# Optimization experiments

Measured on AMD Instinct MI355X. Metric: run time of the kernel, lower is better.

Reference implementation:

```python
import jax, jax.numpy as jnp
import numpy as np

B, N, D, H = 16, 576, 768, 8
HD = D // H
SCALE = HD ** -0.5
EPS = 1e-5  # torch LayerNorm default


def _ln(x, g, b):
    mu = jnp.mean(x, axis=-1, keepdims=True)
    var = jnp.mean(jnp.square(x - mu), axis=-1, keepdims=True)
    return (x - mu) * jax.lax.rsqrt(var + EPS) * g + b


def setup_inputs() -> dict:
    key = jax.random.key(0)
    ks = jax.random.split(key, 20)
    s = D ** -0.5
    inp = {
        "x1": jax.random.normal(ks[0], (B, N, D), jnp.float32),
        "x2": jax.random.normal(ks[1], (B, N, D), jnp.float32),
        # projection weights stored [in, out]
        "Wq": jax.random.normal(ks[2], (D, D), jnp.float32) * s,
        "bq": jnp.zeros((D,), jnp.float32),
        "Wk": jax.random.normal(ks[3], (D, D), jnp.float32) * s,
        "bk": jnp.zeros((D,), jnp.float32),
        "Wv": jax.random.normal(ks[4], (D, D), jnp.float32) * s,
        "bv": jnp.zeros((D,), jnp.float32),
        "Wo": jax.random.normal(ks[5], (D, D), jnp.float32) * s,
        "bo": jnp.zeros((D,), jnp.float32),
        "g1": jnp.ones((D,), jnp.float32),
        "be1": jnp.zeros((D,), jnp.float32),
        "g2": jnp.ones((D,), jnp.float32),
        "be2": jnp.zeros((D,), jnp.float32),
        "W1": jax.random.normal(ks[6], (D, 4 * D), jnp.float32) * s,
        "bf1": jnp.zeros((4 * D,), jnp.float32),
        "W2": jax.random.normal(ks[7], (4 * D, D), jnp.float32) * (4 * D) ** -0.5,
        "bf2": jnp.zeros((D,), jnp.float32),
    }
    return inp


def reference(x1, x2, Wq, bq, Wk, bk, Wv, bv, Wo, bo, g1, be1, g2, be2, W1, bf1, W2, bf2):
    def heads(x, W, b):
        # [B,N,D] -> [B,H,N,HD]
        return (x @ W + b).reshape(B, N, H, HD).transpose(0, 2, 1, 3)

    def block(xq, xkv):
        q = heads(xq, Wq, bq)
        k = heads(xkv, Wk, bk)
        v = heads(xkv, Wv, bv)
        attn = jax.nn.softmax(jnp.einsum('bhqd,bhkd->bhqk', q, k) * SCALE, axis=-1)
        o = jnp.einsum('bhqk,bhkd->bqhd', attn, v).reshape(B, N, D)
        o = o @ Wo + bo
        h = _ln(xq + o, g1, be1)
        f = jax.nn.gelu(h @ W1 + bf1, approximate=False) @ W2 + bf2
        return _ln(h + f, g2, be2), attn

    out1, a1 = block(x1, x2)
    out2, a2 = block(x2, x1)
    attn_map = (a1 + a2.transpose(0, 1, 3, 2)) * 0.5
    return out1, out2, attn_map
```

## Files before the change

kernel.cpp:

```cpp
#include <hip/hip_runtime.h>
#include <cstdint>
#include <cstddef>

#define B_   16
#define N_   576
#define D_   768
#define H_   8
#define HD_  96
#define DF_  3072
#define R_   (B_*N_)
#define SCALE_F 0.10206207261596575f

typedef __bf16 bf16;
typedef __attribute__((ext_vector_type(8))) __bf16 bf16x8;
typedef __attribute__((ext_vector_type(4))) __bf16 bf16x4;
typedef __attribute__((ext_vector_type(4))) float  f32x4;

__device__ __forceinline__ void gld_lds16(const void* g, void* l) {
  __builtin_amdgcn_global_load_lds((const __attribute__((address_space(1))) void*)g,
                                   (__attribute__((address_space(3))) void*)l,
                                   16, 0, 0);
}
__device__ __forceinline__ void nt_f32(float* p, float v) { __builtin_nontemporal_store(v, p); }
__device__ __forceinline__ void nt_u64(void* p, unsigned long long v) { __builtin_nontemporal_store(v, (unsigned long long*)p); }
__device__ __forceinline__ void nt_bf16(bf16* p, float v) {
  bf16 h = (bf16)v; unsigned short u; __builtin_memcpy(&u, &h, 2);
  __builtin_nontemporal_store(u, (unsigned short*)p);
}
__device__ __forceinline__ float gelu_f(float v) {
  float u = 0.7978845608028654f * v * (1.0f + 0.044715f*v*v);
  float e = __expf(2.0f*u);
  float th = 1.0f - 2.0f/(e + 1.0f);
  return 0.5f*v*(1.0f + th);
}

__global__ void cast_f32_bf16_k(const float* __restrict__ x, bf16* __restrict__ y, int n4) {
  int i = blockIdx.x*256 + threadIdx.x;
  if (i >= n4) return;
  f32x4 v = ((const f32x4*)x)[i];
  union { bf16 h[4]; unsigned long long q; } u;
  u.h[0] = (bf16)v[0]; u.h[1] = (bf16)v[1]; u.h[2] = (bf16)v[2]; u.h[3] = (bf16)v[3];
  nt_u64((unsigned long long*)y + i, u.q);
}

__global__ void transpose_cast_k(const float* __restrict__ W, bf16* __restrict__ WT,
                                 int rows, int cols) {
  __shared__ float tile[32][33];
  int cb = blockIdx.x*32, rb = blockIdx.y*32;
  int tx = threadIdx.x, ty = threadIdx.y;
  #pragma unroll
  for (int i=0;i<32;i+=8)
    tile[ty+i][tx] = W[(size_t)(rb+ty+i)*cols + cb+tx];
  __syncthreads();
  #pragma unroll
  for (int i=0;i<32;i+=8)
    WT[(size_t)(cb+ty+i)*rows + rb+tx] = (bf16)tile[tx][ty+i];
}

__global__ void concat_bias_k(const float* a, const float* b, const float* c, float* o) {
  int i = blockIdx.x*256 + threadIdx.x;
  if (i < 768) o[i] = a[i];
  else if (i < 1536) o[i] = b[i-768];
  else if (i < 2304) o[i] = c[i-1536];
}

template<int EPI, int SWZ>
__global__ __launch_bounds__(512, 2) void gemm256_k(
    const bf16* __restrict__ A, const bf16* __restrict__ Bt,
    const float* __restrict__ bias,
    bf16* __restrict__ outB, bf16* __restrict__ outK, bf16* __restrict__ outVT,
    int Nn, int K, int nct)
{
  __shared__ __align__(16) char lds[65536];
  const int t = threadIdx.x;
  const int lane = t & 63, w = t >> 6, g = lane >> 4, r = lane & 15;
  const int wr = w >> 2, wc = w & 3;

  const int cpx = gridDim.x >> 3;
  const int xcd = blockIdx.x & 7, loc = blockIdx.x >> 3;
  int rt, ct;
  if (SWZ) {
    const int nrt_x = cpx / nct;
    ct = loc / nrt_x;
    rt = xcd * nrt_x + (loc - ct*nrt_x);
  } else {
    const int wg = xcd*cpx + loc;
    rt = wg / nct; ct = wg - rt*nct;
  }
  const size_t a0 = (size_t)rt*256, b0 = (size_t)ct*256;

  f32x4 acc[8][4];
  #pragma unroll
  for (int m=0;m<8;++m)
    #pragma unroll
    for (int n=0;n<4;++n) acc[m][n] = (f32x4){0.f,0.f,0.f,0.f};

  const int rbase = ((t>>6)<<4) + (t&15);
  const int kbase = ((t>>4)&3)*8;
  const bf16* Ab = A  + (a0 + rbase)*(size_t)K + kbase;
  const bf16* Bb = Bt + (b0 + rbase)*(size_t)K + kbase;
  const size_t rstep = (size_t)128*K;
  char* Al = lds + t*16;
  char* Bl = lds + 32768 + t*16;

#define STAGE256(tt, cc) do { \
    const size_t ko_ = (size_t)(tt)*32; \
    gld_lds16(Ab + ko_,         Al + (cc)*16384); \
    gld_lds16(Ab + rstep + ko_, Al + (cc)*16384 + 8192); \
    gld_lds16(Bb + ko_,         Bl + (cc)*16384); \
    gld_lds16(Bb + rstep + ko_, Bl + (cc)*16384 + 8192); \
  } while (0)

  const int NT = K >> 5;
  STAGE256(0, 0);
  for (int tt = 0; tt < NT; ++tt) {
    const int c = tt & 1;
    if (tt + 1 < NT) {
      STAGE256(tt + 1, c ^ 1);
      asm volatile("s_waitcnt vmcnt(4)" ::: "memory");
    } else {
      asm volatile("s_waitcnt vmcnt(0)" ::: "memory");
    }
    __builtin_amdgcn_sched_barrier(0);
    __builtin_amdgcn_s_barrier();
    __builtin_amdgcn_sched_barrier(0);

    const char* Ard = lds + c*16384 + (wr<<13) + lane*16;
    const char* Brd = lds + 32768 + c*16384 + (wc<<12) + lane*16;
    bf16x8 bfr[4], af[4];
    #pragma unroll
    for (int n=0;n<4;++n) bfr[n] = *(const bf16x8*)(Brd + n*1024);
    #pragma unroll
    for (int m=0;m<4;++m) af[m]  = *(const bf16x8*)(Ard + m*1024);
    __builtin_amdgcn_s_setprio(1);
    #pragma unroll
    for (int m=0;m<4;++m)
      #pragma unroll
      for (int n=0;n<4;++n)
        acc[m][n] = __builtin_amdgcn_mfma_f32_16x16x32_bf16(af[m], bfr[n], acc[m][n], 0, 0, 0);
    __builtin_amdgcn_s_setprio(0);
    #pragma unroll
    for (int m=0;m<4;++m) af[m] = *(const bf16x8*)(Ard + (4+m)*1024);
    __builtin_amdgcn_s_setprio(1);
    #pragma unroll
    for (int m=0;m<4;++m)
      #pragma unroll
      for (int n=0;n<4;++n)
        acc[4+m][n] = __builtin_amdgcn_mfma_f32_16x16x32_bf16(af[m], bfr[n], acc[4+m][n], 0, 0, 0);
    __builtin_amdgcn_s_setprio(0);
    __builtin_amdgcn_sched_barrier(0);
    __builtin_amdgcn_s_barrier();
    __builtin_amdgcn_sched_barrier(0);
  }
#undef STAGE256

  const int rowb = rt*256;
  const int colb = ct*256;
  bf16* lds16p = (bf16*)lds;
  const int g4 = g*4;
  const bool vtile = (EPI == 4) && (ct >= 6);

  #pragma unroll
  for (int ph = 0; ph < 2; ++ph) {
    __builtin_amdgcn_s_barrier();
    #pragma unroll
    for (int n = 0; n < 4; ++n) {
      const int col = wc*64 + n*16 + r;
      const float bc = bias[colb + col];
      #pragma unroll
      for (int m = 0; m < 4; ++m) {
        #pragma unroll
        for (int j = 0; j < 4; ++j) {
          float v = acc[ph*4+m][n][j] + bc;
          if (EPI == 3) v = gelu_f(v);
          const int rowin = m*16 + g4 + j;
          if (vtile) {
            lds16p[col*128 + wr*64 + (rowin ^ ((col&7)<<3))] = (bf16)v;
          } else {
            const int rowL = wr*64 + rowin;
            const int chs = ((col>>3) ^ ((rowL>>2)&7));
            lds16p[rowL*256 + (chs<<3) + (col&7)] = (bf16)v;
          }
        }
      }
    }
    __builtin_amdgcn_s_barrier();
    if (vtile) {
      #pragma unroll
      for (int i = 0; i < 8; ++i) {
        const int cid = i*512 + t;
        const int col = cid >> 4, chunk = cid & 15, run = chunk >> 3, k = chunk & 7;
        bf16x8 val = *(const bf16x8*)&lds16p[col*128 + run*64 + ((k ^ (col&7))<<3)];
        const int rowg = rowb + run*128 + ph*64 + k*8;
        const int s  = rowg >= R_;
        const int rr = rowg - s*R_;
        const int bb = rr / N_, nn = rr - bb*N_;
        bf16* p = outVT + (size_t)s*R_*D_ + ((size_t)bb*D_ + (ct-6)*256 + col)*N_ + nn;
        __builtin_nontemporal_store(val, (bf16x8*)p);
      }
    } else {
      #pragma unroll
      for (int i = 0; i < 8; ++i) {
        const int cid = i*512 + t;
        const int rl = cid >> 5, ch = cid & 31;
        bf16x8 val = *(const bf16x8*)&lds16p[rl*256 + ((ch ^ ((rl>>2)&7))<<3)];
        const int rowg = rowb + (rl>>6)*128 + ph*64 + (rl&63);
        const int c0 = colb + ch*8;
        if (EPI == 0 || EPI == 3) {
          __builtin_nontemporal_store(val, (bf16x8*)(outB + (size_t)rowg*Nn + c0));
        } else {
          const int s  = rowg >= R_;
          const int rr = rowg - s*R_;
          const int bb = rr / N_, nn = rr - bb*N_;
          const size_t so = (size_t)s*R_*D_;
          bf16* p;
          if (c0 < 768) {
            const int hh = c0/96, dd = c0 - hh*96;
            p = outB + so + ((size_t)(bb*H_+hh)*N_ + nn)*HD_ + dd;
          } else {
            const int c1 = c0 - 768;
            const int hh = c1/96, dd = c1 - hh*96;
            p = outK + so + ((size_t)(bb*H_+hh)*N_ + nn)*HD_ + dd;
          }
          __builtin_nontemporal_store(val, (bf16x8*)p);
        }
      }
    }
  }
}


__global__ __launch_bounds__(256, 2) void attn_stats_k(
    const bf16* __restrict__ Q, const bf16* __restrict__ Kb,
    const bf16* __restrict__ VT, bf16* __restrict__ obuf,
    float* __restrict__ mrow, float* __restrict__ rrow)
{
  __shared__ __align__(16) char plds[2*18432 + 512];
  float* smax = (float*)(plds + 36864);
  float* ssum = smax + 64;
  const int t = threadIdx.x, w = t>>6, lane = t&63, g = lane>>4, r = lane&15;
  const int wq = w>>1, wc = w&1;
  const int h = blockIdx.x & 7, ii = blockIdx.x >> 3;
  const int b = ii/18, qt = ii - b*18, bh = b*8 + h;
  const int q0 = qt*32 + wq*16, c0 = wc*288, row4 = g*4;

  f32x4 s[18];
  #pragma unroll
  for (int n=0;n<18;++n) s[n] = (f32x4){0.f,0.f,0.f,0.f};
  bf16x8 aq[3];
  const bf16* qrow = Q + ((size_t)(b*H_+h)*N_ + q0 + r)*HD_;
  #pragma unroll
  for (int kk=0;kk<3;++kk) aq[kk] = *(const bf16x8*)(qrow + kk*32 + g*8);
  const bf16* kbase = Kb + ((size_t)(b*H_+h)*N_ + c0 + r)*HD_ + g*8;
  #pragma unroll
  for (int n=0;n<18;++n) {
    const bf16* kr = kbase + (size_t)(n*16)*HD_;
    #pragma unroll
    for (int kk=0;kk<3;++kk)
      s[n] = __builtin_amdgcn_mfma_f32_16x16x32_bf16(aq[kk], *(const bf16x8*)(kr + kk*32), s[n], 0, 0, 0);
  }

  float mx[4], sum[4], rinv[4];
  #pragma unroll
  for (int j=0;j<4;++j) {
    float m = -1e30f;
    #pragma unroll
    for (int n=0;n<18;++n) m = fmaxf(m, s[n][j]);
    #pragma unroll
    for (int d=1; d<16; d<<=1) m = fmaxf(m, __shfl_xor(m, d));
    mx[j] = m;
  }
  if ((lane&15)==0) {
    #pragma unroll
    for (int j=0;j<4;++j) smax[(wq*2+wc)*16 + row4+j] = mx[j];
  }
  __syncthreads();
  #pragma unroll
  for (int j=0;j<4;++j) {
    mx[j] = fmaxf(mx[j], smax[(wq*2+(wc^1))*16 + row4+j]);
    sum[j] = 0.f;
  }
  #pragma unroll
  for (int n=0;n<18;++n)
    #pragma unroll
    for (int j=0;j<4;++j) {
      float p = __expf((s[n][j] - mx[j]) * SCALE_F);
      s[n][j] = p; sum[j] += p;
    }
  #pragma unroll
  for (int j=0;j<4;++j) {
    #pragma unroll
    for (int d=1; d<16; d<<=1) sum[j] += __shfl_xor(sum[j], d);
  }
  if ((lane&15)==0) {
    #pragma unroll
    for (int j=0;j<4;++j) ssum[(wq*2+wc)*16 + row4+j] = sum[j];
  }
  __syncthreads();
  #pragma unroll
  for (int j=0;j<4;++j)
    rinv[j] = 1.0f / (sum[j] + ssum[(wq*2+(wc^1))*16 + row4+j]);

  if (wc==0 && (lane&15)==0) {
    const size_t sb = (size_t)bh*N_ + q0 + row4;
    #pragma unroll
    for (int j=0;j<4;++j) { mrow[sb+j] = mx[j]; rrow[sb+j] = rinv[j]; }
  }

  char* pw = plds + wq*18432;
  #pragma unroll
  for (int n=0;n<18;++n)
    #pragma unroll
    for (int j=0;j<4;++j) {
      int kc = c0 + n*16 + r, row = row4 + j;
      *(bf16*)(pw + ((kc>>3)<<8) + (row<<4) + ((kc&7)<<1)) = (bf16)(s[n][j]*rinv[j]);
    }
  __syncthreads();

  f32x4 oa[3];
  #pragma unroll
  for (int n=0;n<3;++n) oa[n] = (f32x4){0.f,0.f,0.f,0.f};
  const bf16* vtb = VT + ((size_t)b*D_ + h*HD_ + wc*48 + r)*N_ + g*8;
  for (int kt=0; kt<18; ++kt) {
    bf16x8 pa = *(const bf16x8*)(pw + kt*1024 + lane*16);
    #pragma unroll
    for (int n=0;n<3;++n)
      oa[n] = __builtin_amdgcn_mfma_f32_16x16x32_bf16(pa, *(const bf16x8*)(vtb + (size_t)(n*16)*N_ + kt*32), oa[n], 0, 0, 0);
  }
  #pragma unroll
  for (int n=0;n<3;++n)
    #pragma unroll
    for (int j=0;j<4;++j)
      nt_bf16(obuf + ((size_t)b*N_ + q0+row4+j)*D_ + h*HD_ + wc*48 + n*16 + r, oa[n][j]);
}

__global__ __launch_bounds__(256, 2) void attn_map_k(
    const bf16* __restrict__ Q1, const bf16* __restrict__ K2,
    const bf16* __restrict__ VT2, const bf16* __restrict__ K1,
    const bf16* __restrict__ Q2, const float* __restrict__ mrow,
    const float* __restrict__ rrow, float* __restrict__ attn_out,
    bf16* __restrict__ obuf)
{
  __shared__ __align__(16) char plds[2*18432 + 512];
  float* smax = (float*)(plds + 36864);
  float* ssum = smax + 64;
  const int t = threadIdx.x, w = t>>6, lane = t&63, g = lane>>4, r = lane&15;
  const int wq = w>>1, wc = w&1;
  const int h = blockIdx.x & 7, ii = blockIdx.x >> 3;
  const int b = ii/18, qt = ii - b*18, bh = b*8 + h;
  const int q0 = qt*32 + wq*16, c0 = wc*288, row4 = g*4;

  f32x4 s[18];
  #pragma unroll
  for (int n=0;n<18;++n) s[n] = (f32x4){0.f,0.f,0.f,0.f};
  bf16x8 aq[3];
  const bf16* qrow = Q1 + ((size_t)(b*H_+h)*N_ + q0 + r)*HD_;
  #pragma unroll
  for (int kk=0;kk<3;++kk) aq[kk] = *(const bf16x8*)(qrow + kk*32 + g*8);
  const bf16* kbase = K2 + ((size_t)(b*H_+h)*N_ + c0 + r)*HD_ + g*8;
  #pragma unroll
  for (int n=0;n<18;++n) {
    const bf16* kr = kbase + (size_t)(n*16)*HD_;
    #pragma unroll
    for (int kk=0;kk<3;++kk)
      s[n] = __builtin_amdgcn_mfma_f32_16x16x32_bf16(aq[kk], *(const bf16x8*)(kr + kk*32), s[n], 0, 0, 0);
  }

  float mx[4], sum[4], rinv[4];
  #pragma unroll
  for (int j=0;j<4;++j) {
    float m = -1e30f;
    #pragma unroll
    for (int n=0;n<18;++n) m = fmaxf(m, s[n][j]);
    #pragma unroll
    for (int d=1; d<16; d<<=1) m = fmaxf(m, __shfl_xor(m, d));
    mx[j] = m;
  }
  if ((lane&15)==0) {
    #pragma unroll
    for (int j=0;j<4;++j) smax[(wq*2+wc)*16 + row4+j] = mx[j];
  }
  __syncthreads();
  #pragma unroll
  for (int j=0;j<4;++j) {
    mx[j] = fmaxf(mx[j], smax[(wq*2+(wc^1))*16 + row4+j]);
    sum[j] = 0.f;
  }
  #pragma unroll
  for (int n=0;n<18;++n)
    #pragma unroll
    for (int j=0;j<4;++j) {
      float p = __expf((s[n][j] - mx[j]) * SCALE_F);
      s[n][j] = p; sum[j] += p;
    }
  #pragma unroll
  for (int j=0;j<4;++j) {
    #pragma unroll
    for (int d=1; d<16; d<<=1) sum[j] += __shfl_xor(sum[j], d);
  }
  if ((lane&15)==0) {
    #pragma unroll
    for (int j=0;j<4;++j) ssum[(wq*2+wc)*16 + row4+j] = sum[j];
  }
  __syncthreads();
  #pragma unroll
  for (int j=0;j<4;++j)
    rinv[j] = 1.0f / (sum[j] + ssum[(wq*2+(wc^1))*16 + row4+j]);

  char* pw = plds + wq*18432;
  #pragma unroll
  for (int n=0;n<18;++n)
    #pragma unroll
    for (int j=0;j<4;++j) {
      int kc = c0 + n*16 + r, row = row4 + j;
      *(bf16*)(pw + ((kc>>3)<<8) + (row<<4) + ((kc&7)<<1)) = (bf16)(s[n][j]*rinv[j]);
    }
  __syncthreads();

  f32x4 oa[3];
  #pragma unroll
  for (int n=0;n<3;++n) oa[n] = (f32x4){0.f,0.f,0.f,0.f};
  const bf16* vtb = VT2 + ((size_t)b*D_ + h*HD_ + wc*48 + r)*N_ + g*8;
  for (int kt=0; kt<18; ++kt) {
    bf16x8 pa = *(const bf16x8*)(pw + kt*1024 + lane*16);
    #pragma unroll
    for (int n=0;n<3;++n)
      oa[n] = __builtin_amdgcn_mfma_f32_16x16x32_bf16(pa, *(const bf16x8*)(vtb + (size_t)(n*16)*N_ + kt*32), oa[n], 0, 0, 0);
  }
  #pragma unroll
  for (int n=0;n<3;++n)
    #pragma unroll
    for (int j=0;j<4;++j)
      nt_bf16(obuf + ((size_t)b*N_ + q0+row4+j)*D_ + h*HD_ + wc*48 + n*16 + r, oa[n][j]);

  #pragma unroll
  for (int n=0;n<18;++n) s[n] = (f32x4){0.f,0.f,0.f,0.f};
  bf16x8 ak[3];
  const bf16* k1row = K1 + ((size_t)(b*H_+h)*N_ + q0 + r)*HD_;
  #pragma unroll
  for (int kk=0;kk<3;++kk) ak[kk] = *(const bf16x8*)(k1row + kk*32 + g*8);
  const bf16* q2b = Q2 + ((size_t)(b*H_+h)*N_ + c0 + r)*HD_ + g*8;
  #pragma unroll
  for (int n=0;n<18;++n) {
    const bf16* qr2 = q2b + (size_t)(n*16)*HD_;
    #pragma unroll
    for (int kk=0;kk<3;++kk)
      s[n] = __builtin_amdgcn_mfma_f32_16x16x32_bf16(ak[kk], *(const bf16x8*)(qr2 + kk*32), s[n], 0, 0, 0);
  }

  const float* mb = mrow + (size_t)bh*N_;
  const float* rb = rrow + (size_t)bh*N_;
  float* aout = attn_out + (size_t)bh*N_*N_;
  #pragma unroll
  for (int n=0;n<18;++n) {
    const int kc = c0 + n*16 + r;
    const float m2v = mb[kc];
    const float rv  = rb[kc];
    #pragma unroll
    for (int j=0;j<4;++j) {
      const int row = row4 + j;
      float p1 = (float)(*(const bf16*)(pw + ((kc>>3)<<8) + (row<<4) + ((kc&7)<<1)));
      float a2t = __expf((s[n][j] - m2v) * SCALE_F) * rv;
      nt_f32(aout + (size_t)(q0 + row)*N_ + kc, 0.5f*(p1 + a2t));
    }
  }
}

template<int MODE>
__global__ __launch_bounds__(256) void ln_k(
    const float* __restrict__ xf1, const float* __restrict__ xf2,
    const bf16* __restrict__ xb, const bf16* __restrict__ y,
    const float* __restrict__ gamma, const float* __restrict__ beta,
    bf16* __restrict__ out16, float* __restrict__ out32)
{
  const int w = threadIdx.x>>6, lane = threadIdx.x&63;
  const size_t row = (size_t)blockIdx.x*4 + w;
  float v[12]; float s = 0.f, s2 = 0.f;
  const bf16* yr = y + row*D_;
  #pragma unroll
  for (int i=0;i<3;++i) {
    int c = i*256 + lane*4;
    bf16x4 bb = *(const bf16x4*)(yr + c);
    float xr4[4];
    if (MODE == 0) {
      const float* xr = (row < R_) ? (xf1 + row*D_) : (xf2 + (row-R_)*D_);
      f32x4 a = *(const f32x4*)(xr + c);
      #pragma unroll
      for (int q=0;q<4;++q) xr4[q] = a[q];
    } else {
      bf16x4 a = *(const bf16x4*)(xb + row*D_ + c);
      #pragma unroll
      for (int q=0;q<4;++q) xr4[q] = (float)a[q];
    }
    #pragma unroll
    for (int q=0;q<4;++q) {
      float tq = xr4[q] + (float)bb[q];
      v[i*4+q] = tq; s += tq; s2 += tq*tq;
    }
  }
  #pragma unroll
  for (int d=1; d<64; d<<=1) { s += __shfl_xor(s, d); s2 += __shfl_xor(s2, d); }
  const float mean = s*(1.f/D_);
  const float var  = s2*(1.f/D_) - mean*mean;
  const float rstd = rsqrtf(var + 1e-5f);
  #pragma unroll
  for (int i=0;i<3;++i) {
    int c = i*256 + lane*4;
    f32x4 gm = *(const f32x4*)(gamma + c);
    f32x4 bt = *(const f32x4*)(beta  + c);
    float o[4];
    #pragma unroll
    for (int q=0;q<4;++q) o[q] = (v[i*4+q]-mean)*rstd*gm[q] + bt[q];
    if (MODE == 0) {
      union { bf16 h[4]; unsigned long long q64; } u;
      u.h[0]=(bf16)o[0]; u.h[1]=(bf16)o[1]; u.h[2]=(bf16)o[2]; u.h[3]=(bf16)o[3];
      nt_u64(out16 + row*D_ + c, u.q64);
    } else {
      f32x4 ov = {o[0], o[1], o[2], o[3]};
      __builtin_nontemporal_store(ov, (f32x4*)(out32 + row*D_ + c));
    }
  }
}

extern "C" void kernel_launch(void* const* d_in, const int* in_sizes, int n_in,
                              void* d_out, int out_size, void* d_ws, size_t ws_size,
                              hipStream_t stream)
{
  const float* x1  = (const float*)d_in[0];
  const float* x2  = (const float*)d_in[1];
  const float* Wq  = (const float*)d_in[2];  const float* bq  = (const float*)d_in[3];
  const float* Wk  = (const float*)d_in[4];  const float* bk  = (const float*)d_in[5];
  const float* Wv  = (const float*)d_in[6];  const float* bv  = (const float*)d_in[7];
  const float* Wo  = (const float*)d_in[8];  const float* bo  = (const float*)d_in[9];
  const float* g1  = (const float*)d_in[10]; const float* be1 = (const float*)d_in[11];
  const float* g2  = (const float*)d_in[12]; const float* be2 = (const float*)d_in[13];
  const float* W1  = (const float*)d_in[14]; const float* bf1 = (const float*)d_in[15];
  const float* W2  = (const float*)d_in[16]; const float* bf2 = (const float*)d_in[17];

  float* outLN = (float*)d_out;
  float* attn  = outLN + (size_t)2*R_*D_;

  char* ws = (char*)d_ws;
  size_t off = 0;
  auto alloc = [&](size_t bytes) -> void* {
    void* p = ws + off;
    off += (bytes + 255) & ~(size_t)255;
    return p;
  };
  const size_t RD2 = (size_t)R_*D_*2;
  size_t span1 = off;
  bf16* xb  = (bf16*)alloc(2*RD2);
  bf16* Qb  = (bf16*)alloc(2*RD2);
  bf16* Kb  = (bf16*)alloc(2*RD2);
  bf16* VTb = (bf16*)alloc(2*RD2);
  bf16* G   = (bf16*)(ws + span1);
  bf16* wqkvT = (bf16*)alloc((size_t)2304*D_*2);
  float* bqkv = (float*)alloc(2304*4);
  bf16* woT   = (bf16*)alloc((size_t)D_*D_*2);
  bf16* w1T   = (bf16*)alloc((size_t)D_*DF_*2);
  bf16* w2T   = (bf16*)alloc((size_t)DF_*D_*2);
  bf16* obuf  = (bf16*)alloc(2*RD2);
  bf16* oprojB= (bf16*)alloc(2*RD2);
  bf16* h16   = (bf16*)alloc(2*RD2);
  bf16* f16   = (bf16*)alloc(2*RD2);
  float* m2r  = (float*)alloc((size_t)B_*H_*N_*4);
  float* r2r  = (float*)alloc((size_t)B_*H_*N_*4);
  (void)ws_size; (void)in_sizes; (void)n_in; (void)out_size;

  const int n4 = R_*D_/4;
  cast_f32_bf16_k<<<n4/256, 256, 0, stream>>>(x1, xb, n4);
  cast_f32_bf16_k<<<n4/256, 256, 0, stream>>>(x2, xb + (size_t)R_*D_, n4);

  dim3 tb(32,8);
  transpose_cast_k<<<dim3(24,24), tb, 0, stream>>>(Wq, wqkvT,             D_, D_);
  transpose_cast_k<<<dim3(24,24), tb, 0, stream>>>(Wk, wqkvT + 768*D_,    D_, D_);
  transpose_cast_k<<<dim3(24,24), tb, 0, stream>>>(Wv, wqkvT + 1536*D_,   D_, D_);
  transpose_cast_k<<<dim3(24,24), tb, 0, stream>>>(Wo, woT, D_, D_);
  transpose_cast_k<<<dim3(96,24), tb, 0, stream>>>(W1, w1T, D_, DF_);
  transpose_cast_k<<<dim3(24,96), tb, 0, stream>>>(W2, w2T, DF_, D_);
  concat_bias_k<<<9, 256, 0, stream>>>(bq, bk, bv, bqkv);

  gemm256_k<4,1><<<648, 512, 0, stream>>>(xb, wqkvT, bqkv, Qb, Kb, VTb, 2304, 768, 9);

  const size_t SD = (size_t)R_*D_;
  attn_stats_k<<<2304, 256, 0, stream>>>(Qb + SD, Kb, VTb, obuf + SD, m2r, r2r);
  attn_map_k  <<<2304, 256, 0, stream>>>(Qb, Kb + SD, VTb + SD, Kb, Qb + SD, m2r, r2r, attn, obuf);

  gemm256_k<0,1><<<216, 512, 0, stream>>>(obuf, woT, bo, oprojB, nullptr, nullptr, 768, 768, 3);
  ln_k<0><<<2*R_/4, 256, 0, stream>>>(x1, x2, nullptr, oprojB, g1, be1, h16, nullptr);
  gemm256_k<3,1><<<864, 512, 0, stream>>>(h16, w1T, bf1, G, nullptr, nullptr, 3072, 768, 12);
  gemm256_k<0,0><<<216, 512, 0, stream>>>(G, w2T, bf2, f16, nullptr, nullptr, 768, 3072, 3);
  ln_k<1><<<2*R_/4, 256, 0, stream>>>(nullptr, nullptr, h16, f16, g2, be2, nullptr, outLN);
}
```

Before: 776.2 us.

## Software-pipeline V loads in PV loops and interleave transposed QK with PV

In both attention kernels the PV loop now prefetches the next V^T fragment into registers one iteration ahead, and the first fragment is issued before the barrier. In the attn_map kernel the transposed K1·Q2 score MFMAs, which used to run as a separate loop after PV, are merged into the PV loop with their Q2 loads prefetched too. The aim is to hide global-load latency behind MFMA work and give the scheduler independent matrix ops to overlap. The cost is higher register pressure from the extra prefetch buffers and the fully unrolled loops, which could hurt occupancy at launch bounds of 2.

Measured after the change: 800.8 us. +3.2%, slower.

```diff
diff --git a/kernel.cpp b/kernel.cpp
--- a/kernel.cpp
+++ b/kernel.cpp
@@ -315,17 +315,29 @@
       int kc = c0 + n*16 + r, row = row4 + j;
       *(bf16*)(pw + ((kc>>3)<<8) + (row<<4) + ((kc&7)<<1)) = (bf16)(s[n][j]*rinv[j]);
     }
+
+  const bf16* vtb = VT + ((size_t)b*D_ + h*HD_ + wc*48 + r)*N_ + g*8;
+  bf16x8 vb[3];
+  #pragma unroll
+  for (int n=0;n<3;++n) vb[n] = *(const bf16x8*)(vtb + (size_t)(n*16)*N_);
   __syncthreads();
 
   f32x4 oa[3];
   #pragma unroll
   for (int n=0;n<3;++n) oa[n] = (f32x4){0.f,0.f,0.f,0.f};
-  const bf16* vtb = VT + ((size_t)b*D_ + h*HD_ + wc*48 + r)*N_ + g*8;
+  #pragma unroll
   for (int kt=0; kt<18; ++kt) {
     bf16x8 pa = *(const bf16x8*)(pw + kt*1024 + lane*16);
+    bf16x8 nxt[3];
+    if (kt < 17) {
+      #pragma unroll
+      for (int n=0;n<3;++n) nxt[n] = *(const bf16x8*)(vtb + (size_t)(n*16)*N_ + (kt+1)*32);
+    }
     #pragma unroll
     for (int n=0;n<3;++n)
-      oa[n] = __builtin_amdgcn_mfma_f32_16x16x32_bf16(pa, *(const bf16x8*)(vtb + (size_t)(n*16)*N_ + kt*32), oa[n], 0, 0, 0);
+      oa[n] = __builtin_amdgcn_mfma_f32_16x16x32_bf16(pa, vb[n], oa[n], 0, 0, 0);
+    #pragma unroll
+    for (int n=0;n<3;++n) vb[n] = nxt[n];
   }
   #pragma unroll
   for (int n=0;n<3;++n)
@@ -415,38 +427,52 @@
       int kc = c0 + n*16 + r, row = row4 + j;
       *(bf16*)(pw + ((kc>>3)<<8) + (row<<4) + ((kc&7)<<1)) = (bf16)(s[n][j]*rinv[j]);
     }
+
+  bf16x8 ak[3];
+  const bf16* k1row = K1 + ((size_t)(b*H_+h)*N_ + q0 + r)*HD_;
+  #pragma unroll
+  for (int kk=0;kk<3;++kk) ak[kk] = *(const bf16x8*)(k1row + kk*32 + g*8);
+  const bf16* vtb = VT2 + ((size_t)b*D_ + h*HD_ + wc*48 + r)*N_ + g*8;
+  const bf16* q2b = Q2 + ((size_t)(b*H_+h)*N_ + c0 + r)*HD_ + g*8;
+  bf16x8 vb[3], qb[3];
+  #pragma unroll
+  for (int n=0;n<3;++n) vb[n] = *(const bf16x8*)(vtb + (size_t)(n*16)*N_);
+  #pragma unroll
+  for (int kk=0;kk<3;++kk) qb[kk] = *(const bf16x8*)(q2b + kk*32);
   __syncthreads();
 
   f32x4 oa[3];
   #pragma unroll
   for (int n=0;n<3;++n) oa[n] = (f32x4){0.f,0.f,0.f,0.f};
-  const bf16* vtb = VT2 + ((size_t)b*D_ + h*HD_ + wc*48 + r)*N_ + g*8;
-  for (int kt=0; kt<18; ++kt) {
-    bf16x8 pa = *(const bf16x8*)(pw + kt*1024 + lane*16);
+  #pragma unroll
+  for (int i=0; i<18; ++i) {
+    bf16x8 pa = *(const bf16x8*)(pw + i*1024 + lane*16);
+    bf16x8 nv[3], nq[3];
+    if (i < 17) {
+      #pragma unroll
+      for (int n=0;n<3;++n) nv[n] = *(const bf16x8*)(vtb + (size_t)(n*16)*N_ + (i+1)*32);
+      #pragma unroll
+      for (int kk=0;kk<3;++kk) nq[kk] = *(const bf16x8*)(q2b + (size_t)((i+1)*16)*HD_ + kk*32);
+    }
     #pragma unroll
     for (int n=0;n<3;++n)
-      oa[n] = __builtin_amdgcn_mfma_f32_16x16x32_bf16(pa, *(const bf16x8*)(vtb + (size_t)(n*16)*N_ + kt*32), oa[n], 0, 0, 0);
-  }
+      oa[n] = __builtin_amdgcn_mfma_f32_16x16x32_bf16(pa, vb[n], oa[n], 0, 0, 0);
+    f32x4 tacc = (f32x4){0.f,0.f,0.f,0.f};
+    #pragma unroll
+    for (int kk=0;kk<3;++kk)
+      tacc = __builtin_amdgcn_mfma_f32_16x16x32_bf16(ak[kk], qb[kk], tacc, 0, 0, 0);
+    s[i] = tacc;
+    #pragma unroll
+    for (int n=0;n<3;++n) vb[n] = nv[n];
+    #pragma unroll
+    for (int kk=0;kk<3;++kk) qb[kk] = nq[kk];
+  }
+
   #pragma unroll
   for (int n=0;n<3;++n)
     #pragma unroll
     for (int j=0;j<4;++j)
       nt_bf16(obuf + ((size_t)b*N_ + q0+row4+j)*D_ + h*HD_ + wc*48 + n*16 + r, oa[n][j]);
-
-  #pragma unroll
-  for (int n=0;n<18;++n) s[n] = (f32x4){0.f,0.f,0.f,0.f};
-  bf16x8 ak[3];
-  const bf16* k1row = K1 + ((size_t)(b*H_+h)*N_ + q0 + r)*HD_;
-  #pragma unroll
-  for (int kk=0;kk<3;++kk) ak[kk] = *(const bf16x8*)(k1row + kk*32 + g*8);
-  const bf16* q2b = Q2 + ((size_t)(b*H_+h)*N_ + c0 + r)*HD_ + g*8;
-  #pragma unroll
-  for (int n=0;n<18;++n) {
-    const bf16* qr2 = q2b + (size_t)(n*16)*HD_;
-    #pragma unroll
-    for (int kk=0;kk<3;++kk)
-      s[n] = __builtin_amdgcn_mfma_f32_16x16x32_bf16(ak[kk], *(const bf16x8*)(qr2 + kk*32), s[n], 0, 0, 0);
-  }
 
   const float* mb = mrow + (size_t)bh*N_;
   const float* rb = rrow + (size_t)bh*N_;
```

## Replace 256x256 double-buffered GEMM with single-buffered 128x128 tile kernel

Applied to the files above, without the earlier changes.

Swaps the 512-thread 256x256-tile GEMM, which double-buffers K=32 slices, for a 256-thread 128x128-tile GEMM. The new kernel loads K=64 slices into a single LDS buffer with a __syncthreads before and after the compute. The aim is more workgroups per launch, giving better CU fill and load balance on the smaller GEMMs. The cost is lower operand reuse per tile, more global/L2 traffic, and no overlap between loads and MFMA compute.

Measured after the change: 917.2 us. 18.2% more time.

```diff
diff --git a/kernel.cpp b/kernel.cpp
--- a/kernel.cpp
+++ b/kernel.cpp
@@ -65,16 +65,17 @@
 }
 
 template<int EPI, int SWZ>
-__global__ __launch_bounds__(512, 2) void gemm256_k(
+__global__ __launch_bounds__(256, 2) void gemm128_k(
     const bf16* __restrict__ A, const bf16* __restrict__ Bt,
     const float* __restrict__ bias,
     bf16* __restrict__ outB, bf16* __restrict__ outK, bf16* __restrict__ outVT,
     int Nn, int K, int nct)
 {
-  __shared__ __align__(16) char lds[65536];
+  __shared__ __align__(16) char lds[32768];
+  char* As = lds; char* Bs = lds + 16384;
   const int t = threadIdx.x;
   const int lane = t & 63, w = t >> 6, g = lane >> 4, r = lane & 15;
-  const int wr = w >> 2, wc = w & 3;
+  const int wr = w >> 1, wc = w & 1;
 
   const int cpx = gridDim.x >> 3;
   const int xcd = blockIdx.x & 7, loc = blockIdx.x >> 3;
@@ -87,143 +88,110 @@
     const int wg = xcd*cpx + loc;
     rt = wg / nct; ct = wg - rt*nct;
   }
-  const size_t a0 = (size_t)rt*256, b0 = (size_t)ct*256;
-
-  f32x4 acc[8][4];
-  #pragma unroll
-  for (int m=0;m<8;++m)
+  const size_t a0 = (size_t)rt*128, b0 = (size_t)ct*128;
+
+  f32x4 acc[4][4];
+  #pragma unroll
+  for (int m=0;m<4;++m)
     #pragma unroll
     for (int n=0;n<4;++n) acc[m][n] = (f32x4){0.f,0.f,0.f,0.f};
 
-  const int rbase = ((t>>6)<<4) + (t&15);
-  const int kbase = ((t>>4)&3)*8;
-  const bf16* Ab = A  + (a0 + rbase)*(size_t)K + kbase;
-  const bf16* Bb = Bt + (b0 + rbase)*(size_t)K + kbase;
-  const size_t rstep = (size_t)128*K;
-  char* Al = lds + t*16;
-  char* Bl = lds + 32768 + t*16;
-
-#define STAGE256(tt, cc) do { \
-    const size_t ko_ = (size_t)(tt)*32; \
-    gld_lds16(Ab + ko_,         Al + (cc)*16384); \
-    gld_lds16(Ab + rstep + ko_, Al + (cc)*16384 + 8192); \
-    gld_lds16(Bb + ko_,         Bl + (cc)*16384); \
-    gld_lds16(Bb + rstep + ko_, Bl + (cc)*16384 + 8192); \
-  } while (0)
-
-  const int NT = K >> 5;
-  STAGE256(0, 0);
-  for (int tt = 0; tt < NT; ++tt) {
-    const int c = tt & 1;
-    if (tt + 1 < NT) {
-      STAGE256(tt + 1, c ^ 1);
-      asm volatile("s_waitcnt vmcnt(4)" ::: "memory");
-    } else {
-      asm volatile("s_waitcnt vmcnt(0)" ::: "memory");
-    }
-    __builtin_amdgcn_sched_barrier(0);
-    __builtin_amdgcn_s_barrier();
-    __builtin_amdgcn_sched_barrier(0);
-
-    const char* Ard = lds + c*16384 + (wr<<13) + lane*16;
-    const char* Brd = lds + 32768 + c*16384 + (wc<<12) + lane*16;
-    bf16x8 bfr[4], af[4];
-    #pragma unroll
-    for (int n=0;n<4;++n) bfr[n] = *(const bf16x8*)(Brd + n*1024);
-    #pragma unroll
-    for (int m=0;m<4;++m) af[m]  = *(const bf16x8*)(Ard + m*1024);
-    __builtin_amdgcn_s_setprio(1);
-    #pragma unroll
-    for (int m=0;m<4;++m)
+  const int k8    = (t>>4)&7;
+  const int rbase = ((t>>7)<<4) + (t&15);
+  const bf16* Abase = A  + (a0 + rbase)*(size_t)K + k8*8;
+  const bf16* Bbase = Bt + (b0 + rbase)*(size_t)K + k8*8;
+  const size_t rstep = (size_t)32*K;
+  const int nkb = K >> 6;
+
+  for (int kb = 0; kb < nkb; ++kb) {
+    const size_t ko = (size_t)kb*64;
+    #pragma unroll
+    for (int i=0;i<4;++i) {
+      gld_lds16(Abase + (size_t)i*rstep + ko, As + i*4096 + t*16);
+      gld_lds16(Bbase + (size_t)i*rstep + ko, Bs + i*4096 + t*16);
+    }
+    __syncthreads();
+    #pragma unroll
+    for (int kk=0;kk<2;++kk) {
+      bf16x8 af[4], bfr[4];
       #pragma unroll
-      for (int n=0;n<4;++n)
-        acc[m][n] = __builtin_amdgcn_mfma_f32_16x16x32_bf16(af[m], bfr[n], acc[m][n], 0, 0, 0);
-    __builtin_amdgcn_s_setprio(0);
-    #pragma unroll
-    for (int m=0;m<4;++m) af[m] = *(const bf16x8*)(Ard + (4+m)*1024);
-    __builtin_amdgcn_s_setprio(1);
-    #pragma unroll
-    for (int m=0;m<4;++m)
+      for (int m=0;m<4;++m) af[m]  = *(const bf16x8*)(As + (wr*4+m)*2048 + kk*1024 + lane*16);
       #pragma unroll
-      for (int n=0;n<4;++n)
-        acc[4+m][n] = __builtin_amdgcn_mfma_f32_16x16x32_bf16(af[m], bfr[n], acc[4+m][n], 0, 0, 0);
-    __builtin_amdgcn_s_setprio(0);
-    __builtin_amdgcn_sched_barrier(0);
-    __builtin_amdgcn_s_barrier();
-    __builtin_amdgcn_sched_barrier(0);
-  }
-#undef STAGE256
-
-  const int rowb = rt*256;
-  const int colb = ct*256;
+      for (int n=0;n<4;++n) bfr[n] = *(const bf16x8*)(Bs + (wc*4+n)*2048 + kk*1024 + lane*16);
+      #pragma unroll
+      for (int m=0;m<4;++m)
+        #pragma unroll
+        for (int n=0;n<4;++n)
+          acc[m][n] = __builtin_amdgcn_mfma_f32_16x16x32_bf16(af[m], bfr[n], acc[m][n], 0, 0, 0);
+    }
+    __syncthreads();
+  }
+
+  const int rowb = rt*128;
+  const int colb = ct*128;
   bf16* lds16p = (bf16*)lds;
-  const int g4 = g*4;
-  const bool vtile = (EPI == 4) && (ct >= 6);
-
-  #pragma unroll
-  for (int ph = 0; ph < 2; ++ph) {
-    __builtin_amdgcn_s_barrier();
-    #pragma unroll
-    for (int n = 0; n < 4; ++n) {
-      const int col = wc*64 + n*16 + r;
-      const float bc = bias[colb + col];
+  const bool vtile = (EPI == 4) && (ct >= 12);
+
+  #pragma unroll
+  for (int n = 0; n < 4; ++n) {
+    const int col = wc*64 + n*16 + r;
+    const float bc = bias[colb + col];
+    #pragma unroll
+    for (int m = 0; m < 4; ++m) {
       #pragma unroll
-      for (int m = 0; m < 4; ++m) {
-        #pragma unroll
-        for (int j = 0; j < 4; ++j) {
-          float v = acc[ph*4+m][n][j] + bc;
-          if (EPI == 3) v = gelu_f(v);
-          const int rowin = m*16 + g4 + j;
-          if (vtile) {
-            lds16p[col*128 + wr*64 + (rowin ^ ((col&7)<<3))] = (bf16)v;
-          } else {
-            const int rowL = wr*64 + rowin;
-            const int chs = ((col>>3) ^ ((rowL>>2)&7));
-            lds16p[rowL*256 + (chs<<3) + (col&7)] = (bf16)v;
-          }
+      for (int j = 0; j < 4; ++j) {
+        float v = acc[m][n][j] + bc;
+        if (EPI == 3) v = gelu_f(v);
+        const int rowL = wr*64 + m*16 + g*4 + j;
+        if (vtile) {
+          lds16p[col*128 + (rowL ^ ((col&7)<<3))] = (bf16)v;
+        } else {
+          const int chs = ((col>>3) ^ ((rowL>>2)&7));
+          lds16p[rowL*128 + (chs<<3) + (col&7)] = (bf16)v;
         }
       }
     }
-    __builtin_amdgcn_s_barrier();
-    if (vtile) {
-      #pragma unroll
-      for (int i = 0; i < 8; ++i) {
-        const int cid = i*512 + t;
-        const int col = cid >> 4, chunk = cid & 15, run = chunk >> 3, k = chunk & 7;
-        bf16x8 val = *(const bf16x8*)&lds16p[col*128 + run*64 + ((k ^ (col&7))<<3)];
-        const int rowg = rowb + run*128 + ph*64 + k*8;
+  }
+  __syncthreads();
+  if (vtile) {
+    #pragma unroll
+    for (int i = 0; i < 8; ++i) {
+      const int cid = i*256 + t;
+      const int colL = cid >> 4, k = cid & 15;
+      bf16x8 val = *(const bf16x8*)&lds16p[colL*128 + ((k ^ (colL&7))<<3)];
+      const int rowg = rowb + k*8;
+      const int s  = rowg >= R_;
+      const int rr = rowg - s*R_;
+      const int bb = rr / N_, nn = rr - bb*N_;
+      const int dglob = (ct-12)*128 + colL;
+      bf16* p = outVT + (size_t)s*R_*D_ + ((size_t)bb*D_ + dglob)*N_ + nn;
+      __builtin_nontemporal_store(val, (bf16x8*)p);
+    }
+  } else {
+    #pragma unroll
+    for (int i = 0; i < 8; ++i) {
+      const int cid = i*256 + t;
+      const int rl = cid >> 4, ch = cid & 15;
+      bf16x8 val = *(const bf16x8*)&lds16p[rl*128 + ((ch ^ ((rl>>2)&7))<<3)];
+      const int rowg = rowb + rl;
+      const int c0 = colb + ch*8;
+      if (EPI == 0 || EPI == 3) {
+        __builtin_nontemporal_store(val, (bf16x8*)(outB + (size_t)rowg*Nn + c0));
+      } else {
         const int s  = rowg >= R_;
         const int rr = rowg - s*R_;
         const int bb = rr / N_, nn = rr - bb*N_;
-        bf16* p = outVT + (size_t)s*R_*D_ + ((size_t)bb*D_ + (ct-6)*256 + col)*N_ + nn;
+        const size_t so = (size_t)s*R_*D_;
+        bf16* p;
+        if (c0 < 768) {
+          const int hh = c0/96, dd = c0 - hh*96;
+          p = outB + so + ((size_t)(bb*H_+hh)*N_ + nn)*HD_ + dd;
+        } else {
+          const int c1 = c0 - 768;
+          const int hh = c1/96, dd = c1 - hh*96;
+          p = outK + so + ((size_t)(bb*H_+hh)*N_ + nn)*HD_ + dd;
+        }
         __builtin_nontemporal_store(val, (bf16x8*)p);
-      }
-    } else {
-      #pragma unroll
-      for (int i = 0; i < 8; ++i) {
-        const int cid = i*512 + t;
-        const int rl = cid >> 5, ch = cid & 31;
-        bf16x8 val = *(const bf16x8*)&lds16p[rl*256 + ((ch ^ ((rl>>2)&7))<<3)];
-        const int rowg = rowb + (rl>>6)*128 + ph*64 + (rl&63);
-        const int c0 = colb + ch*8;
-        if (EPI == 0 || EPI == 3) {
-          __builtin_nontemporal_store(val, (bf16x8*)(outB + (size_t)rowg*Nn + c0));
-        } else {
-          const int s  = rowg >= R_;
-          const int rr = rowg - s*R_;
-          const int bb = rr / N_, nn = rr - bb*N_;
-          const size_t so = (size_t)s*R_*D_;
-          bf16* p;
-          if (c0 < 768) {
-            const int hh = c0/96, dd = c0 - hh*96;
-            p = outB + so + ((size_t)(bb*H_+hh)*N_ + nn)*HD_ + dd;
-          } else {
-            const int c1 = c0 - 768;
-            const int hh = c1/96, dd = c1 - hh*96;
-            p = outK + so + ((size_t)(bb*H_+hh)*N_ + nn)*HD_ + dd;
-          }
-          __builtin_nontemporal_store(val, (bf16x8*)p);
-        }
       }
     }
   }
@@ -580,15 +548,15 @@
   transpose_cast_k<<<dim3(24,96), tb, 0, stream>>>(W2, w2T, DF_, D_);
   concat_bias_k<<<9, 256, 0, stream>>>(bq, bk, bv, bqkv);
 
-  gemm256_k<4,1><<<648, 512, 0, stream>>>(xb, wqkvT, bqkv, Qb, Kb, VTb, 2304, 768, 9);
+  gemm128_k<4,1><<<2592, 256, 0, stream>>>(xb, wqkvT, bqkv, Qb, Kb, VTb, 2304, 768, 18);
 
   const size_t SD = (size_t)R_*D_;
   attn_stats_k<<<2304, 256, 0, stream>>>(Qb + SD, Kb, VTb, obuf + SD, m2r, r2r);
   attn_map_k  <<<2304, 256, 0, stream>>>(Qb, Kb + SD, VTb + SD, Kb, Qb + SD, m2r, r2r, attn, obuf);
 
-  gemm256_k<0,1><<<216, 512, 0, stream>>>(obuf, woT, bo, oprojB, nullptr, nullptr, 768, 768, 3);
+  gemm128_k<0,1><<<864, 256, 0, stream>>>(obuf, woT, bo, oprojB, nullptr, nullptr, 768, 768, 6);
   ln_k<0><<<2*R_/4, 256, 0, stream>>>(x1, x2, nullptr, oprojB, g1, be1, h16, nullptr);
-  gemm256_k<3,1><<<864, 512, 0, stream>>>(h16, w1T, bf1, G, nullptr, nullptr, 3072, 768, 12);
-  gemm256_k<0,0><<<216, 512, 0, stream>>>(G, w2T, bf2, f16, nullptr, nullptr, 768, 3072, 3);
+  gemm128_k<3,1><<<3456, 256, 0, stream>>>(h16, w1T, bf1, G, nullptr, nullptr, 3072, 768, 24);
+  gemm128_k<0,0><<<864, 256, 0, stream>>>(G, w2T, bf2, f16, nullptr, nullptr, 768, 3072, 6);
   ln_k<1><<<2*R_/4, 256, 0, stream>>>(nullptr, nullptr, h16, f16, g2, be2, nullptr, outLN);
 }
```
